# Kernel optimization log

Measured on AMD Instinct MI355X. Metric: run time of the kernel, lower is better.

## Reference

```python
import jax, jax.numpy as jnp
import numpy as np

D, ED, N, R, K, NL = 128, 256, 16, 8, 4, 3   # d_model, d_inner, d_state, dt_rank, d_conv, n_layers
B, L = 4, 1024
HID, OUT = 256, 2
EPS = 1e-5


def setup_inputs() -> dict:
    key = jax.random.key(0)
    ks = jax.random.split(key, 16)
    g = lambda k, shape, s=0.05: jax.random.normal(k, shape, dtype=jnp.float32) * s
    return {
        "x": jax.random.normal(ks[0], (B, L, D), dtype=jnp.float32),
        # Mamba params, stacked over (2 directions, NL layers)
        "rms_w": jnp.ones((2, NL, D), jnp.float32),
        "in_w": g(ks[1], (2, NL, 2 * ED, D)),
        "in_b": g(ks[2], (2, NL, 2 * ED)),
        "conv_w": g(ks[3], (2, NL, ED, K)),
        "conv_b": g(ks[4], (2, NL, ED)),
        "xproj_w": g(ks[5], (2, NL, R + 2 * N, ED)),
        "dt_w": g(ks[6], (2, NL, ED, R)),
        "dt_b": g(ks[7], (2, NL, ED)),
        "A_log": jnp.broadcast_to(jnp.log(jnp.arange(1.0, N + 1.0, dtype=jnp.float32)), (2, NL, ED, N)) + 0.0,
        "Dp": jnp.ones((2, NL, ED), jnp.float32),
        "out_w": g(ks[8], (2, NL, D, ED)),
        "out_b": g(ks[9], (2, NL, D)),
        # MLP head params (BatchNorm in training mode: batch stats)
        "bn1_g": jnp.ones((2 * D,), jnp.float32), "bn1_b": jnp.zeros((2 * D,), jnp.float32),
        "w1": g(ks[10], (HID, 2 * D)), "b1": g(ks[11], (HID,)),
        "bn2_g": jnp.ones((HID,), jnp.float32), "bn2_b": jnp.zeros((HID,), jnp.float32),
        "w2": g(ks[12], (HID, HID)), "b2": g(ks[13], (HID,)),
        "bn3_g": jnp.ones((HID,), jnp.float32), "bn3_b": jnp.zeros((HID,), jnp.float32),
        "w3": g(ks[14], (OUT, HID)), "b3": g(ks[15], (OUT,)),
    }


def _rms(x, w):
    return x * jax.lax.rsqrt(jnp.mean(x * x, axis=-1, keepdims=True) + EPS) * w


def _dwconv(x, w, b):
    # causal depthwise conv; x: (B,L,ED), w: (ED,K)
    y = jax.lax.conv_general_dilated(x.transpose(0, 2, 1), w[:, None, :], (1,), [(K - 1, 0)],
                                     feature_group_count=ED, dimension_numbers=("NCH", "OIH", "NCH"))
    return y.transpose(0, 2, 1) + b


def _ssm(dA, dBx, C):
    # dA,dBx: (B,L,ED,N); C: (B,L,N) -> y: (B,L,ED)
    def step(h, inp):
        a, bx, c = inp
        h = a * h + bx
        return h, jnp.einsum("ben,bn->be", h, c)
    h0 = jnp.zeros((dA.shape[0], ED, N), dA.dtype)
    _, ys = jax.lax.scan(step, h0, (dA.transpose(1, 0, 2, 3), dBx.transpose(1, 0, 2, 3), C.transpose(1, 0, 2)))
    return ys.transpose(1, 0, 2)


def _block(x, in_w, in_b, conv_w, conv_b, xproj_w, dt_w, dt_b, A_log, Dp, out_w, out_b):
    xz = x @ in_w.T + in_b
    xi, z = xz[..., :ED], xz[..., ED:]
    xi = jax.nn.silu(_dwconv(xi, conv_w, conv_b))
    dbc = xi @ xproj_w.T
    dt, Bm, Cm = dbc[..., :R], dbc[..., R:R + N], dbc[..., R + N:]
    delta = jax.nn.softplus(dt @ dt_w.T + dt_b)            # (B,L,ED)
    A = -jnp.exp(A_log)                                    # (ED,N)
    dA = jnp.exp(delta[..., None] * A)                     # (B,L,ED,N)
    dBx = (delta * xi)[..., None] * Bm[:, :, None, :]      # (B,L,ED,N)
    y = _ssm(dA, dBx, Cm) + Dp * xi
    y = y * jax.nn.silu(z)
    return y @ out_w.T + out_b


def _mamba(x, d, rms_w, in_w, in_b, conv_w, conv_b, xproj_w, dt_w, dt_b, A_log, Dp, out_w, out_b):
    for l in range(NL):
        x = x + _block(_rms(x, rms_w[d, l]), in_w[d, l], in_b[d, l], conv_w[d, l], conv_b[d, l],
                       xproj_w[d, l], dt_w[d, l], dt_b[d, l], A_log[d, l], Dp[d, l], out_w[d, l], out_b[d, l])
    return x


def _bn(x, g, b):
    m = jnp.mean(x, axis=0)
    v = jnp.mean((x - m) ** 2, axis=0)  # biased var, torch BN training mode
    return (x - m) * jax.lax.rsqrt(v + EPS) * g + b


def _forward(x, rms_w, in_w, in_b, conv_w, conv_b, xproj_w, dt_w, dt_b, A_log, Dp, out_w, out_b,
             bn1_g, bn1_b, w1, b1, bn2_g, bn2_b, w2, b2, bn3_g, bn3_b, w3, b3):
    mp = (rms_w, in_w, in_b, conv_w, conv_b, xproj_w, dt_w, dt_b, A_log, Dp, out_w, out_b)
    fwd = _mamba(x, 0, *mp)
    bwd = jnp.flip(_mamba(jnp.flip(x, axis=1), 1, *mp), axis=1)
    h = jnp.concatenate([fwd, bwd], axis=2).reshape(B * L, 2 * D)
    h = jax.nn.leaky_relu(_bn(h, bn1_g, bn1_b) @ w1.T + b1)
    h = jax.nn.leaky_relu(_bn(h, bn2_g, bn2_b) @ w2.T + b2)
    h = _bn(h, bn3_g, bn3_b) @ w3.T + b3
    return h.reshape(B, L, OUT)


def reference(x, rms_w, in_w, in_b, conv_w, conv_b, xproj_w, dt_w, dt_b, A_log, Dp, out_w, out_b,
              bn1_g, bn1_b, w1, b1, bn2_g, bn2_b, w2, b2, bn3_g, bn3_b, w3, b3):
    return _forward(x, rms_w, in_w, in_b, conv_w, conv_b, xproj_w, dt_w, dt_b, A_log, Dp, out_w, out_b,
                    bn1_g, bn1_b, w1, b1, bn2_g, bn2_b, w2, b2, bn3_g, bn3_b, w3, b3)
```

## Files before the change

kernel.cpp:

```cpp
#include <hip/hip_runtime.h>
#include <hip/hip_bf16.h>

#define NL 3
#define EPS 1e-5f

#define C_RMSW   0L
#define C_INW    768L
#define C_INB    393984L
#define C_CONVW  397056L
#define C_CONVB  403200L
#define C_XPROJW 404736L
#define C_DTW    466176L
#define C_DTB    478464L
#define C_ALOG   480000L
#define C_DP     504576L
#define C_OUTW   506112L
#define C_OUTB   702720L
#define C_BN1G   703488L
#define C_BN1B   703744L
#define C_W1     704000L
#define C_B1     769536L
#define C_BN2G   769792L
#define C_BN2B   770048L
#define C_W2     770304L
#define C_B2     835840L
#define C_BN3G   836096L
#define C_BN3B   836352L
#define C_W3     836608L
#define C_B3     837120L
#define FLAG_OFF 837184L
#define X0_OFF   837248L
#define X1_OFF   1361536L
#define XZT_OFF  1885824L
#define XCP_OFF  6080128L
#define DBCT_OFF 8177280L
#define YGP_OFF  8504960L
#define BNS_OFF  10602112L
#define H1_OFF   XZT_OFF
#define H2_OFF   (XZT_OFF + 1048576L)

struct Ptrs { const void* p[25]; };

static __device__ const int  CV_SRC[26] = {0,0,1,2,3,4,5,6,7,8,9,10,11,12,13,14,15,16,17,18,19,20,21,22,23,24};
static __device__ const long CV_DST[26] = {X0_OFF,X1_OFF,C_RMSW,C_INW,C_INB,C_CONVW,C_CONVB,C_XPROJW,C_DTW,C_DTB,
                                           C_ALOG,C_DP,C_OUTW,C_OUTB,C_BN1G,C_BN1B,C_W1,C_B1,C_BN2G,C_BN2B,
                                           C_W2,C_B2,C_BN3G,C_BN3B,C_W3,C_B3};
static __device__ const int  CV_SZ[26]  = {524288,524288,768,393216,3072,6144,1536,61440,12288,1536,
                                           24576,1536,196608,768,256,256,65536,256,256,256,
                                           65536,256,256,256,512,2};

__global__ __launch_bounds__(256) void k_convert(Ptrs ps, float* __restrict__ ws) {
  bool isbf = (*(const unsigned int*)ps.p[1]) == 0x3F803F80u;
  if (blockIdx.x == 0 && blockIdx.y == 0 && threadIdx.x == 0) ws[FLAG_OFF] = isbf ? 1.f : 0.f;
  int job = blockIdx.y;
  int n = CV_SZ[job];
  const void* s = ps.p[CV_SRC[job]];
  float* dp = ws + CV_DST[job];
  int stride = gridDim.x * blockDim.x;
  bool permute = (job < 2);
  for (int i = blockIdx.x * blockDim.x + threadIdx.x; i < n; i += stride) {
    long si = i;
    if (permute) {
      int row = i >> 7, col = i & 127;
      int b = row >> 10, p = row & 1023;
      int t = ((p & 63) << 4) + (p >> 6);
      si = ((long)((b << 10) + t) << 7) + col;
    }
    float v;
    if (isbf) {
      unsigned int u = ((const unsigned short*)s)[si];
      v = __uint_as_float(u << 16);
    } else {
      v = ((const float*)s)[si];
    }
    dp[i] = v;
  }
}

#define ASLD 68

__device__ inline void mm_inner(const float* As, const float* Bs, float4* acc) {
  int tx = threadIdx.x & 15, ty = threadIdx.x >> 4;
  #pragma unroll
  for (int k = 0; k < 64; ++k) {
    float4 av = *(const float4*)&As[k*ASLD + ty*4];
    float4 bv = *(const float4*)&Bs[k*ASLD + tx*4];
    acc[0].x = fmaf(av.x,bv.x,acc[0].x); acc[0].y = fmaf(av.x,bv.y,acc[0].y); acc[0].z = fmaf(av.x,bv.z,acc[0].z); acc[0].w = fmaf(av.x,bv.w,acc[0].w);
    acc[1].x = fmaf(av.y,bv.x,acc[1].x); acc[1].y = fmaf(av.y,bv.y,acc[1].y); acc[1].z = fmaf(av.y,bv.z,acc[1].z); acc[1].w = fmaf(av.y,bv.w,acc[1].w);
    acc[2].x = fmaf(av.z,bv.x,acc[2].x); acc[2].y = fmaf(av.z,bv.y,acc[2].y); acc[2].z = fmaf(av.z,bv.z,acc[2].z); acc[2].w = fmaf(av.z,bv.w,acc[2].w);
    acc[3].x = fmaf(av.w,bv.x,acc[3].x); acc[3].y = fmaf(av.w,bv.y,acc[3].y); acc[3].z = fmaf(av.w,bv.z,acc[3].z); acc[3].w = fmaf(av.w,bv.w,acc[3].w);
  }
}

__device__ inline void stageT_g(float* S, const float* src, int ld, int row0, int k0, int nvalid) {
  int m = threadIdx.x >> 2, q = threadIdx.x & 3;
  const float* p = src + (long)(row0 + m) * ld + k0 + q*16;
  bool ok = (row0 + m) < nvalid;
  #pragma unroll
  for (int j = 0; j < 4; ++j) {
    float4 v = ok ? *(const float4*)(p + j*4) : make_float4(0.f,0.f,0.f,0.f);
    int kk = q*16 + j*4;
    S[(kk+0)*ASLD+m] = v.x; S[(kk+1)*ASLD+m] = v.y; S[(kk+2)*ASLD+m] = v.z; S[(kk+3)*ASLD+m] = v.w;
  }
}

__device__ inline void stageD(float* S, const float* srcT, long ld, int m0, int k0) {
  int k = threadIdx.x >> 2, q = threadIdx.x & 3;
  const float* p = srcT + (long)(k0 + k) * ld + m0 + q*16;
  float4 v0 = *(const float4*)(p);
  float4 v1 = *(const float4*)(p+4);
  float4 v2 = *(const float4*)(p+8);
  float4 v3 = *(const float4*)(p+12);
  float* s = &S[k*ASLD + q*16];
  *(float4*)(s)    = v0; *(float4*)(s+4)  = v1; *(float4*)(s+8)  = v2; *(float4*)(s+12) = v3;
}

__global__ __launch_bounds__(256) void k1_rms_inproj(float* __restrict__ ws, int layer) {
  int d = blockIdx.z, mt = blockIdx.x, nt = blockIdx.y;
  const float* X  = ws + (d ? X1_OFF : X0_OFF);
  const float* W  = ws + C_INW + (long)((d*NL+layer)*512) * 128;
  const float* Rw = ws + C_RMSW + (d*NL+layer)*128;
  const float* Bi = ws + C_INB + (d*NL+layer)*512;
  __shared__ float As[64*ASLD];
  __shared__ float Bs[64*ASLD];
  __shared__ float rsq[64][4];
  __shared__ float rsc[64];
  int tx = threadIdx.x & 15, ty = threadIdx.x >> 4;
  float4 acc[4] = {make_float4(0,0,0,0),make_float4(0,0,0,0),make_float4(0,0,0,0),make_float4(0,0,0,0)};
  float sq = 0.f;
  for (int kt = 0; kt < 2; ++kt) {
    int k0 = kt * 64;
    {
      int m = threadIdx.x >> 2, q = threadIdx.x & 3;
      const float* p  = X + (long)(mt*64 + m) * 128 + k0 + q*16;
      const float* rw = Rw + k0 + q*16;
      #pragma unroll
      for (int j = 0; j < 4; ++j) {
        float4 v = *(const float4*)(p + j*4);
        float4 r = *(const float4*)(rw + j*4);
        sq += v.x*v.x + v.y*v.y + v.z*v.z + v.w*v.w;
        int kk = q*16 + j*4;
        As[(kk+0)*ASLD+m] = v.x*r.x; As[(kk+1)*ASLD+m] = v.y*r.y;
        As[(kk+2)*ASLD+m] = v.z*r.z; As[(kk+3)*ASLD+m] = v.w*r.w;
      }
    }
    stageT_g(Bs, W, 128, nt*64, k0, 512);
    __syncthreads();
    mm_inner(As, Bs, acc);
    __syncthreads();
  }
  { int m = threadIdx.x >> 2, q = threadIdx.x & 3; rsq[m][q] = sq; }
  __syncthreads();
  if (threadIdx.x < 64) {
    float s = rsq[threadIdx.x][0] + rsq[threadIdx.x][1] + rsq[threadIdx.x][2] + rsq[threadIdx.x][3];
    rsc[threadIdx.x] = rsqrtf(s * (1.f/128.f) + EPS);
  }
  __syncthreads();
  int n0 = tx*4;
  float4 bb = *(const float4*)&Bi[nt*64 + n0];
  const float* bbp = (const float*)&bb;
  #pragma unroll
  for (int i = 0; i < 4; ++i) {
    int m = ty*4 + i;
    float r = rsc[m];
    const float* av = (const float*)&acc[i];
    #pragma unroll
    for (int cc = 0; cc < 4; ++cc) {
      As[(n0+cc)*65 + m] = av[cc]*r + bbp[cc];
    }
  }
  __syncthreads();
  float* xzt = ws + XZT_OFF + (long)d*2097152L + (long)(nt*64)*4096 + mt*64;
  #pragma unroll
  for (int r = 0; r < 16; ++r) {
    int el = r*256 + threadIdx.x;
    int row = el >> 6, m = el & 63;
    xzt[(long)row*4096 + m] = As[row*65 + m];
  }
}

__global__ __launch_bounds__(256) void k2_conv(float* __restrict__ ws, int layer) {
  int e = blockIdx.x, d = blockIdx.y;
  const float* xrow = ws + XZT_OFF + (long)d*2097152L + (long)e*4096;
  float* orow = ws + XCP_OFF + (long)d*1048576L + (long)e*4096;
  __shared__ float s1[4*1040];
  __shared__ float s2[4*1040];
  int tid = threadIdx.x;
  #pragma unroll
  for (int r = 0; r < 16; ++r) {
    int g = r*256 + tid;
    int b = g >> 10, p = g & 1023;
    int s = (p >> 6)*65 + (p & 63);
    s1[b*1040 + s] = xrow[g];
  }
  __syncthreads();
  float4 wv = *(const float4*)(ws + C_CONVW + (long)((d*NL+layer)*256 + e) * 4);
  float cb = ws[C_CONVB + (d*NL+layer)*256 + e];
  #pragma unroll
  for (int r = 0; r < 16; ++r) {
    int tg = r*256 + tid;
    int b = tg >> 10, tl = tg & 1023;
    const float* st = s1 + b*1040;
    #define SIDX(t) (((t)&15)*65 + ((t)>>4))
    float a = cb;
    if (d == 0) {
      float x0 = (tl >= 3) ? st[SIDX(tl-3)] : 0.f;
      float x1 = (tl >= 2) ? st[SIDX(tl-2)] : 0.f;
      float x2 = (tl >= 1) ? st[SIDX(tl-1)] : 0.f;
      float x3 = st[SIDX(tl)];
      a += wv.x*x0 + wv.y*x1 + wv.z*x2 + wv.w*x3;
    } else {
      float x0 = (tl <= 1020) ? st[SIDX(tl+3)] : 0.f;
      float x1 = (tl <= 1021) ? st[SIDX(tl+2)] : 0.f;
      float x2 = (tl <= 1022) ? st[SIDX(tl+1)] : 0.f;
      float x3 = st[SIDX(tl)];
      a += wv.x*x0 + wv.y*x1 + wv.z*x2 + wv.w*x3;
    }
    #undef SIDX
    s2[b*1040 + ((tl & 15)*65 + (tl >> 4))] = a / (1.f + __expf(-a));
  }
  __syncthreads();
  #pragma unroll
  for (int r = 0; r < 16; ++r) {
    int g = r*256 + tid;
    int b = g >> 10, p = g & 1023;
    orow[g] = s2[b*1040 + (p >> 6)*65 + (p & 63)];
  }
}

__global__ __launch_bounds__(256) void k3_xproj(float* __restrict__ ws, int layer) {
  int d = blockIdx.z, mt = blockIdx.x;
  int m0 = mt * 64;
  const float* srcT = ws + XCP_OFF + (long)d*1048576L;
  const float* W = ws + C_XPROJW + (long)((d*NL+layer)*40) * 256;
  __shared__ float As[64*ASLD];
  __shared__ float Bs[64*ASLD];
  float4 acc[4] = {make_float4(0,0,0,0),make_float4(0,0,0,0),make_float4(0,0,0,0),make_float4(0,0,0,0)};
  for (int kt = 0; kt < 4; ++kt) {
    stageD(As, srcT, 4096L, m0, kt*64);
    stageT_g(Bs, W, 256, 0, kt*64, 40);
    __syncthreads();
    mm_inner(As, Bs, acc);
    __syncthreads();
  }
  int tx = threadIdx.x & 15, ty = threadIdx.x >> 4;
  #pragma unroll
  for (int i = 0; i < 4; ++i) {
    const float* av = (const float*)&acc[i];
    #pragma unroll
    for (int cc = 0; cc < 4; ++cc) {
      Bs[(tx*4+cc)*65 + ty*4+i] = av[cc];
    }
  }
  __syncthreads();
  float* dbcT = ws + DBCT_OFF + (long)d*163840L;
  #pragma unroll
  for (int r = 0; r < 10; ++r) {
    int el = r*256 + threadIdx.x;
    int n = el >> 6, m = el & 63;
    dbcT[(long)n*4096 + m0 + m] = Bs[n*65 + m];
  }
}

__device__ inline float softplusf(float x) {
  if (x > 20.f) return x;
  return __logf(1.f + __expf(x));
}

__global__ __launch_bounds__(256) void k5_scan(float* __restrict__ ws, int layer) {
  int d = blockIdx.z, b = blockIdx.y, eg = blockIdx.x;
  int es = threadIdx.x >> 6;
  int c  = threadIdx.x & 63;
  int e = eg*4 + es;
  int g0 = b*1024 + c;
  const float* xcp = ws + XCP_OFF + (long)d*1048576L + (long)e*4096 + g0;
  const float* zp  = ws + XZT_OFF + (long)d*2097152L + (long)(256+e)*4096 + g0;
  const float* dbc = ws + DBCT_OFF + (long)d*163840L + g0;
  float*       yo  = ws + YGP_OFF + (long)d*1048576L + (long)e*4096 + g0;
  const float* dw = ws + C_DTW + (long)((d*NL+layer)*256 + e)*8;
  float dtb = ws[C_DTB + (d*NL+layer)*256 + e];
  const float* al = ws + C_ALOG + (long)((d*NL+layer)*256 + e)*16;
  float Dpe = ws[C_DP + (d*NL+layer)*256 + e];
  float dtw[8];
  #pragma unroll
  for (int n = 0; n < 8; ++n) dtw[n] = dw[n];
  float Anv[16]; bool fast = true;
  #pragma unroll
  for (int n = 0; n < 16; ++n) {
    Anv[n] = -__expf(al[n]);
    fast = fast && (fabsf(Anv[n] + (float)(n+1)) < 1e-3f * (float)(n+1));
  }
  __shared__ float aL[4*64*17];
  __shared__ float hL[4*64*17];
  float h[16], ap[16], del[16], xcv[16];
  float Q = 1.f;
  #pragma unroll
  for (int n = 0; n < 16; ++n) { h[n] = 0.f; ap[n] = 1.f; }
  int i0 = d ? 15 : 0, di = d ? -1 : 1;
  for (int s = 0; s < 16; ++s) {
    int i = i0 + s*di;
    int off = i*64;
    float a0 = dtb;
    #pragma unroll
    for (int n = 0; n < 8; ++n) a0 += dbc[(long)n*4096 + off] * dtw[n];
    float dl = softplusf(a0);
    float xc = xcp[off];
    del[s] = dl; xcv[s] = xc;
    float dx = dl * xc;
    if (fast) {
      float q = __expf(-dl);
      float qp[16];
      qp[0]=q; qp[1]=q*q; qp[2]=qp[1]*q; qp[3]=qp[1]*qp[1];
      float q4=qp[3];
      qp[4]=qp[0]*q4; qp[5]=qp[1]*q4; qp[6]=qp[2]*q4; qp[7]=q4*q4;
      float q8=qp[7];
      #pragma unroll
      for (int j = 0; j < 8; ++j) qp[8+j]=qp[j]*q8;
      Q *= q;
      #pragma unroll
      for (int n = 0; n < 16; ++n)
        h[n] = fmaf(qp[n], h[n], dx * dbc[(long)(8+n)*4096 + off]);
    } else {
      #pragma unroll
      for (int n = 0; n < 16; ++n) {
        float a = __expf(dl * Anv[n]);
        ap[n] *= a;
        h[n] = fmaf(a, h[n], dx * dbc[(long)(8+n)*4096 + off]);
      }
    }
  }
  if (fast) {
    float p = Q;
    #pragma unroll
    for (int n = 0; n < 16; ++n) { ap[n] = p; p *= Q; }
  }
  int base = (es*64 + c)*17;
  #pragma unroll
  for (int n = 0; n < 16; ++n) { aL[base+n] = ap[n]; hL[base+n] = h[n]; }
  __syncthreads();
  if (threadIdx.x < 64) {
    int e2 = threadIdx.x >> 4, n = threadIdx.x & 15;
    float h0 = 0.f;
    for (int s2 = 0; s2 < 64; ++s2) {
      int cc = d ? (63 - s2) : s2;
      int ix = (e2*64 + cc)*17 + n;
      float ta = aL[ix], th = hL[ix];
      aL[ix] = h0;
      h0 = fmaf(ta, h0, th);
    }
  }
  __syncthreads();
  #pragma unroll
  for (int n = 0; n < 16; ++n) h[n] = aL[base+n];
  for (int s = 0; s < 16; ++s) {
    int i = i0 + s*di;
    int off = i*64;
    float dl = del[s], xc = xcv[s];
    float dx = dl * xc;
    float zr = zp[off];
    float zg = zr / (1.f + __expf(-zr));
    float ya[4] = {0.f,0.f,0.f,0.f};
    if (fast) {
      float q = __expf(-dl);
      float qp[16];
      qp[0]=q; qp[1]=q*q; qp[2]=qp[1]*q; qp[3]=qp[1]*qp[1];
      float q4=qp[3];
      qp[4]=qp[0]*q4; qp[5]=qp[1]*q4; qp[6]=qp[2]*q4; qp[7]=q4*q4;
      float q8=qp[7];
      #pragma unroll
      for (int j = 0; j < 8; ++j) qp[8+j]=qp[j]*q8;
      #pragma unroll
      for (int n = 0; n < 16; ++n) {
        h[n] = fmaf(qp[n], h[n], dx * dbc[(long)(8+n)*4096 + off]);
        ya[n & 3] = fmaf(h[n], dbc[(long)(24+n)*4096 + off], ya[n & 3]);
      }
    } else {
      #pragma unroll
      for (int n = 0; n < 16; ++n) {
        float a = __expf(dl * Anv[n]);
        h[n] = fmaf(a, h[n], dx * dbc[(long)(8+n)*4096 + off]);
        ya[n & 3] = fmaf(h[n], dbc[(long)(24+n)*4096 + off], ya[n & 3]);
      }
    }
    float y = (ya[0] + ya[1]) + (ya[2] + ya[3]);
    y = fmaf(Dpe, xc, y);
    yo[off] = y * zg;
  }
}

__global__ __launch_bounds__(256) void k6_outproj(float* __restrict__ ws, int layer) {
  int d = blockIdx.z, mt = blockIdx.x, nt = blockIdx.y;
  int m0 = mt * 64;
  const float* srcT = ws + YGP_OFF + (long)d*1048576L;
  const float* W  = ws + C_OUTW + (long)((d*NL+layer)*128) * 256;
  const float* Ob = ws + C_OUTB + (d*NL+layer)*128;
  float* Xd = ws + (d ? X1_OFF : X0_OFF);
  __shared__ float As[64*ASLD];
  __shared__ float Bs[64*ASLD];
  float4 acc[4] = {make_float4(0,0,0,0),make_float4(0,0,0,0),make_float4(0,0,0,0),make_float4(0,0,0,0)};
  for (int kt = 0; kt < 4; ++kt) {
    stageD(As, srcT, 4096L, m0, kt*64);
    stageT_g(Bs, W, 256, nt*64, kt*64, 128);
    __syncthreads();
    mm_inner(As, Bs, acc);
    __syncthreads();
  }
  int tx = threadIdx.x & 15, ty = threadIdx.x >> 4;
  int n0 = nt*64 + tx*4;
  float4 ob4 = *(const float4*)&Ob[n0];
  #pragma unroll
  for (int i = 0; i < 4; ++i) {
    long tok = (long)m0 + ty*4 + i;
    float4 cur = *(float4*)&Xd[tok*128 + n0];
    float4 v;
    v.x = acc[i].x + ob4.x + cur.x; v.y = acc[i].y + ob4.y + cur.y;
    v.z = acc[i].z + ob4.z + cur.z; v.w = acc[i].w + ob4.w + cur.w;
    *(float4*)&Xd[tok*128 + n0] = v;
  }
}

__global__ __launch_bounds__(256) void bn_stats(float* __restrict__ ws, int stage) {
  int ch = blockIdx.x;
  const float* src; long ld; const float* g; const float* bb;
  if (stage == 0) { src = ws + ((ch < 128) ? (X0_OFF + ch) : (X1_OFF + ch - 128)); ld = 128; g = ws + C_BN1G; bb = ws + C_BN1B; }
  else if (stage == 1) { src = ws + H1_OFF + ch; ld = 256; g = ws + C_BN2G; bb = ws + C_BN2B; }
  else { src = ws + H2_OFF + ch; ld = 256; g = ws + C_BN3G; bb = ws + C_BN3B; }
  float s = 0.f, s2 = 0.f;
  for (int i = threadIdx.x; i < 4096; i += 256) {
    float v = src[(long)i * ld];
    s += v; s2 += v*v;
  }
  #pragma unroll
  for (int o = 32; o > 0; o >>= 1) { s += __shfl_down(s, o, 64); s2 += __shfl_down(s2, o, 64); }
  __shared__ float ls[4], ls2[4];
  int wid = threadIdx.x >> 6, lane = threadIdx.x & 63;
  if (lane == 0) { ls[wid] = s; ls2[wid] = s2; }
  __syncthreads();
  if (threadIdx.x == 0) {
    float S = ls[0]+ls[1]+ls[2]+ls[3], S2 = ls2[0]+ls2[1]+ls2[2]+ls2[3];
    float mean = S * (1.f/4096.f);
    float var = S2 * (1.f/4096.f) - mean*mean;
    float sc = g[ch] * rsqrtf(var + EPS);
    ws[BNS_OFF + stage*512 + ch] = sc;
    ws[BNS_OFF + stage*512 + 256 + ch] = bb[ch] - mean * sc;
  }
}

template<int STAGE>
__global__ __launch_bounds__(256) void hgemm_k(float* __restrict__ ws, void* dout) {
  int mt = blockIdx.x, nt = blockIdx.y;
  const float* sc = ws + BNS_OFF + STAGE*512;
  const float* sh = sc + 256;
  const float* W = ws + (STAGE == 0 ? C_W1 : (STAGE == 1 ? C_W2 : C_W3));
  __shared__ float As[64*ASLD];
  __shared__ float Bs[64*ASLD];
  float4 acc[4] = {make_float4(0,0,0,0),make_float4(0,0,0,0),make_float4(0,0,0,0),make_float4(0,0,0,0)};
  for (int kt = 0; kt < 4; ++kt) {
    int k0 = kt * 64;
    const float* src; int ld;
    if (STAGE == 0) { ld = 128; src = (k0 < 128) ? (ws + X0_OFF + k0) : (ws + X1_OFF + (k0 - 128)); }
    else { ld = 256; src = ws + (STAGE == 1 ? H1_OFF : H2_OFF) + k0; }
    {
      int m = threadIdx.x >> 2, q = threadIdx.x & 3;
      const float* p   = src + (long)(mt*64 + m) * ld + q*16;
      const float* scp = sc + k0 + q*16;
      const float* shp = sh + k0 + q*16;
      #pragma unroll
      for (int j = 0; j < 4; ++j) {
        float4 v  = *(const float4*)(p + j*4);
        float4 s4 = *(const float4*)(scp + j*4);
        float4 h4 = *(const float4*)(shp + j*4);
        int kk = q*16 + j*4;
        As[(kk+0)*ASLD+m] = v.x*s4.x + h4.x; As[(kk+1)*ASLD+m] = v.y*s4.y + h4.y;
        As[(kk+2)*ASLD+m] = v.z*s4.z + h4.z; As[(kk+3)*ASLD+m] = v.w*s4.w + h4.w;
      }
    }
    stageT_g(Bs, W, 256, nt*64, k0, STAGE == 2 ? 2 : 256);
    __syncthreads();
    mm_inner(As, Bs, acc);
    __syncthreads();
  }
  int tx = threadIdx.x & 15, ty = threadIdx.x >> 4;
  if (STAGE == 2) {
    if (tx == 0) {
      bool isbf = ws[FLAG_OFF] != 0.f;
      float b0 = ws[C_B3], b1 = ws[C_B3 + 1];
      #pragma unroll
      for (int i = 0; i < 4; ++i) {
        int r = mt*64 + ty*4 + i;
        int b = r >> 10, p = r & 1023;
        int t = ((p & 63) << 4) + (p >> 6);
        long tok = (long)(b << 10) + t;
        float v0 = acc[i].x + b0, v1 = acc[i].y + b1;
        if (isbf) {
          __hip_bfloat16* o = (__hip_bfloat16*)dout;
          o[tok*2]   = __float2bfloat16(v0);
          o[tok*2+1] = __float2bfloat16(v1);
        } else {
          float* o = (float*)dout;
          o[tok*2] = v0; o[tok*2+1] = v1;
        }
      }
    }
  } else {
    const float* bp = ws + (STAGE == 0 ? C_B1 : C_B2);
    int n0 = nt*64 + tx*4;
    float4 b4 = *(const float4*)&bp[n0];
    float* H = ws + (STAGE == 0 ? H1_OFF : H2_OFF);
    #pragma unroll
    for (int i = 0; i < 4; ++i) {
      long tok = (long)mt*64 + ty*4 + i;
      float4 v;
      v.x = acc[i].x + b4.x; v.y = acc[i].y + b4.y; v.z = acc[i].z + b4.z; v.w = acc[i].w + b4.w;
      v.x = v.x > 0.f ? v.x : 0.01f*v.x;
      v.y = v.y > 0.f ? v.y : 0.01f*v.y;
      v.z = v.z > 0.f ? v.z : 0.01f*v.z;
      v.w = v.w > 0.f ? v.w : 0.01f*v.w;
      *(float4*)&H[tok*256 + n0] = v;
    }
  }
}

extern "C" void kernel_launch(void* const* d_in, const int* in_sizes, int n_in,
                              void* d_out, int out_size, void* d_ws, size_t ws_size,
                              hipStream_t stream) {
  (void)in_sizes; (void)n_in; (void)out_size; (void)ws_size;
  float* ws = (float*)d_ws;
  Ptrs ps;
  for (int i = 0; i < 25; ++i) ps.p[i] = d_in[i];
  k_convert<<<dim3(64, 26), dim3(256), 0, stream>>>(ps, ws);
  for (int l = 0; l < NL; ++l) {
    k1_rms_inproj<<<dim3(64, 8, 2), dim3(256), 0, stream>>>(ws, l);
    k2_conv      <<<dim3(256, 2),   dim3(256), 0, stream>>>(ws, l);
    k3_xproj     <<<dim3(64, 1, 2), dim3(256), 0, stream>>>(ws, l);
    k5_scan      <<<dim3(64, 4, 2), dim3(256), 0, stream>>>(ws, l);
    k6_outproj   <<<dim3(64, 2, 2), dim3(256), 0, stream>>>(ws, l);
  }
  bn_stats<<<dim3(256), dim3(256), 0, stream>>>(ws, 0);
  hgemm_k<0><<<dim3(64, 4), dim3(256), 0, stream>>>(ws, d_out);
  bn_stats<<<dim3(256), dim3(256), 0, stream>>>(ws, 1);
  hgemm_k<1><<<dim3(64, 4), dim3(256), 0, stream>>>(ws, d_out);
  bn_stats<<<dim3(256), dim3(256), 0, stream>>>(ws, 2);
  hgemm_k<2><<<dim3(64, 1), dim3(256), 0, stream>>>(ws, d_out);
}
```

Before: 463.9 us.

## Use fp16 MFMA for projections and fuse BatchNorm stats into GEMM epilogues

The in-projection, out-projection and two MLP head GEMMs now run on fp16 MFMA 16x16x32 instructions instead of scalar fp32 FMA tiles. Weights are pre-converted to fp16 once, with the RMSNorm weight folded into the in-projection weights. BatchNorm batch statistics are accumulated with atomics in the producing GEMM epilogues, which removes the separate bn_stats kernels. In exchange, fp16 rounding of activations and weights reduces accuracy, and variance computed as E[x^2]-mean^2 with float atomics is less stable and not bit-reproducible.

```diff
diff --git a/kernel.cpp b/kernel.cpp
--- a/kernel.cpp
+++ b/kernel.cpp
@@ -1,11 +1,10 @@
 #include <hip/hip_runtime.h>
 #include <hip/hip_bf16.h>
+#include <hip/hip_fp16.h>
 
 #define NL 3
 #define EPS 1e-5f
 
-#define C_RMSW   0L
-#define C_INW    768L
 #define C_INB    393984L
 #define C_CONVW  397056L
 #define C_CONVB  403200L
@@ -14,15 +13,12 @@
 #define C_DTB    478464L
 #define C_ALOG   480000L
 #define C_DP     504576L
-#define C_OUTW   506112L
 #define C_OUTB   702720L
 #define C_BN1G   703488L
 #define C_BN1B   703744L
-#define C_W1     704000L
 #define C_B1     769536L
 #define C_BN2G   769792L
 #define C_BN2B   770048L
-#define C_W2     770304L
 #define C_B2     835840L
 #define C_BN3G   836096L
 #define C_BN3B   836352L
@@ -35,49 +31,77 @@
 #define XCP_OFF  6080128L
 #define DBCT_OFF 8177280L
 #define YGP_OFF  8504960L
-#define BNS_OFF  10602112L
+#define BNA_OFF  10603648L
+#define HINW_OFF  10605184L
+#define HOUTW_OFF 10801792L
+#define HW1_OFF   10900096L
+#define HW2_OFF   10932864L
 #define H1_OFF   XZT_OFF
 #define H2_OFF   (XZT_OFF + 1048576L)
 
+#define ASLD 68
+
 struct Ptrs { const void* p[25]; };
 
-static __device__ const int  CV_SRC[26] = {0,0,1,2,3,4,5,6,7,8,9,10,11,12,13,14,15,16,17,18,19,20,21,22,23,24};
-static __device__ const long CV_DST[26] = {X0_OFF,X1_OFF,C_RMSW,C_INW,C_INB,C_CONVW,C_CONVB,C_XPROJW,C_DTW,C_DTB,
-                                           C_ALOG,C_DP,C_OUTW,C_OUTB,C_BN1G,C_BN1B,C_W1,C_B1,C_BN2G,C_BN2B,
-                                           C_W2,C_B2,C_BN3G,C_BN3B,C_W3,C_B3};
-static __device__ const int  CV_SZ[26]  = {524288,524288,768,393216,3072,6144,1536,61440,12288,1536,
-                                           24576,1536,196608,768,256,256,65536,256,256,256,
-                                           65536,256,256,256,512,2};
-
-__global__ __launch_bounds__(256) void k_convert(Ptrs ps, float* __restrict__ ws) {
+typedef _Float16 half8 __attribute__((ext_vector_type(8)));
+typedef float f32x4 __attribute__((ext_vector_type(4)));
+
+static __device__ const int  CV_SRC[21] = {0,0,3,4,5,6,7,8,9,10,12,13,14,16,17,18,20,21,22,23,24};
+static __device__ const long CV_DST[21] = {X0_OFF,X1_OFF,C_INB,C_CONVW,C_CONVB,C_XPROJW,C_DTW,C_DTB,C_ALOG,C_DP,
+                                           C_OUTB,C_BN1G,C_BN1B,C_B1,C_BN2G,C_BN2B,C_B2,C_BN3G,C_BN3B,C_W3,C_B3};
+static __device__ const int  CV_SZ[21]  = {524288,524288,3072,6144,1536,61440,12288,1536,24576,1536,
+                                           768,256,256,256,256,256,256,256,256,512,2};
+
+__device__ inline float ldsrc(const void* s, long i, bool isbf) {
+  if (isbf) { unsigned int u = ((const unsigned short*)s)[i]; return __uint_as_float(u << 16); }
+  return ((const float*)s)[i];
+}
+
+__global__ __launch_bounds__(256) void g_convert(Ptrs ps, float* __restrict__ ws) {
   bool isbf = (*(const unsigned int*)ps.p[1]) == 0x3F803F80u;
-  if (blockIdx.x == 0 && blockIdx.y == 0 && threadIdx.x == 0) ws[FLAG_OFF] = isbf ? 1.f : 0.f;
   int job = blockIdx.y;
-  int n = CV_SZ[job];
-  const void* s = ps.p[CV_SRC[job]];
-  float* dp = ws + CV_DST[job];
-  int stride = gridDim.x * blockDim.x;
-  bool permute = (job < 2);
-  for (int i = blockIdx.x * blockDim.x + threadIdx.x; i < n; i += stride) {
-    long si = i;
-    if (permute) {
-      int row = i >> 7, col = i & 127;
-      int b = row >> 10, p = row & 1023;
-      int t = ((p & 63) << 4) + (p >> 6);
-      si = ((long)((b << 10) + t) << 7) + col;
-    }
-    float v;
-    if (isbf) {
-      unsigned int u = ((const unsigned short*)s)[si];
-      v = __uint_as_float(u << 16);
-    } else {
-      v = ((const float*)s)[si];
-    }
-    dp[i] = v;
-  }
-}
-
-#define ASLD 68
+  if (job == 0 && blockIdx.x == 0 && threadIdx.x == 0) ws[FLAG_OFF] = isbf ? 1.f : 0.f;
+  int tid0 = blockIdx.x * 256 + threadIdx.x;
+  int stride = gridDim.x * 256;
+  if (job < 21) {
+    int n = CV_SZ[job];
+    const void* s = ps.p[CV_SRC[job]];
+    float* dp = ws + CV_DST[job];
+    bool permute = (job < 2);
+    for (int i = tid0; i < n; i += stride) {
+      long si = i;
+      if (permute) {
+        int row = i >> 7, col = i & 127;
+        int b = row >> 10, p = row & 1023;
+        int t = ((p & 63) << 4) + (p >> 6);
+        si = ((long)((b << 10) + t) << 7) + col;
+      }
+      dp[i] = ldsrc(s, si, isbf);
+    }
+  } else if (job == 21) {
+    _Float16* dp = (_Float16*)(ws + HINW_OFF);
+    const void* sw = ps.p[2]; const void* sr = ps.p[1];
+    for (int i = tid0; i < 393216; i += stride) {
+      int dl = i >> 16, k = i & 127;
+      float v = ldsrc(sw, i, isbf) * ldsrc(sr, dl*128 + k, isbf);
+      dp[i] = (_Float16)v;
+    }
+  } else if (job == 22) {
+    _Float16* dp = (_Float16*)(ws + HOUTW_OFF);
+    const void* s = ps.p[11];
+    for (int i = tid0; i < 196608; i += stride) dp[i] = (_Float16)ldsrc(s, i, isbf);
+  } else if (job == 23) {
+    _Float16* dp = (_Float16*)(ws + HW1_OFF);
+    const void* s = ps.p[15];
+    for (int i = tid0; i < 65536; i += stride) dp[i] = (_Float16)ldsrc(s, i, isbf);
+  } else if (job == 24) {
+    _Float16* dp = (_Float16*)(ws + HW2_OFF);
+    const void* s = ps.p[19];
+    for (int i = tid0; i < 65536; i += stride) dp[i] = (_Float16)ldsrc(s, i, isbf);
+  } else {
+    for (int i = tid0; i < 1536; i += stride) ws[BNA_OFF + i] = 0.f;
+  }
+}
 
 __device__ inline void mm_inner(const float* As, const float* Bs, float4* acc) {
   int tx = threadIdx.x & 15, ty = threadIdx.x >> 4;
@@ -115,71 +139,72 @@
   *(float4*)(s)    = v0; *(float4*)(s+4)  = v1; *(float4*)(s+8)  = v2; *(float4*)(s+12) = v3;
 }
 
-__global__ __launch_bounds__(256) void k1_rms_inproj(float* __restrict__ ws, int layer) {
-  int d = blockIdx.z, mt = blockIdx.x, nt = blockIdx.y;
-  const float* X  = ws + (d ? X1_OFF : X0_OFF);
-  const float* W  = ws + C_INW + (long)((d*NL+layer)*512) * 128;
-  const float* Rw = ws + C_RMSW + (d*NL+layer)*128;
+__device__ inline float softplusf(float x) {
+  if (x > 20.f) return x;
+  return __logf(1.f + __expf(x));
+}
+
+__global__ __launch_bounds__(256) void g_k1m(float* __restrict__ ws, int layer) {
+  int d = blockIdx.z, nt = blockIdx.y, pt = blockIdx.x;
+  const float* X = ws + (d ? X1_OFF : X0_OFF);
+  const _Float16* Wf = (const _Float16*)(ws + HINW_OFF) + (long)(d*NL+layer)*65536;
   const float* Bi = ws + C_INB + (d*NL+layer)*512;
-  __shared__ float As[64*ASLD];
-  __shared__ float Bs[64*ASLD];
-  __shared__ float rsq[64][4];
+  __shared__ float rsq[256];
   __shared__ float rsc[64];
-  int tx = threadIdx.x & 15, ty = threadIdx.x >> 4;
-  float4 acc[4] = {make_float4(0,0,0,0),make_float4(0,0,0,0),make_float4(0,0,0,0),make_float4(0,0,0,0)};
-  float sq = 0.f;
-  for (int kt = 0; kt < 2; ++kt) {
-    int k0 = kt * 64;
-    {
-      int m = threadIdx.x >> 2, q = threadIdx.x & 3;
-      const float* p  = X + (long)(mt*64 + m) * 128 + k0 + q*16;
-      const float* rw = Rw + k0 + q*16;
-      #pragma unroll
-      for (int j = 0; j < 4; ++j) {
-        float4 v = *(const float4*)(p + j*4);
-        float4 r = *(const float4*)(rw + j*4);
-        sq += v.x*v.x + v.y*v.y + v.z*v.z + v.w*v.w;
-        int kk = q*16 + j*4;
-        As[(kk+0)*ASLD+m] = v.x*r.x; As[(kk+1)*ASLD+m] = v.y*r.y;
-        As[(kk+2)*ASLD+m] = v.z*r.z; As[(kk+3)*ASLD+m] = v.w*r.w;
-      }
-    }
-    stageT_g(Bs, W, 128, nt*64, k0, 512);
-    __syncthreads();
-    mm_inner(As, Bs, acc);
-    __syncthreads();
-  }
-  { int m = threadIdx.x >> 2, q = threadIdx.x & 3; rsq[m][q] = sq; }
+  int p0 = pt*64;
+  {
+    int row = threadIdx.x >> 2, q = threadIdx.x & 3;
+    const float* xp = X + (long)(p0+row)*128 + q*32;
+    float s = 0.f;
+    #pragma unroll
+    for (int j = 0; j < 8; ++j) {
+      float4 v = *(const float4*)(xp + j*4);
+      s += v.x*v.x + v.y*v.y + v.z*v.z + v.w*v.w;
+    }
+    rsq[row*4+q] = s;
+  }
   __syncthreads();
   if (threadIdx.x < 64) {
-    float s = rsq[threadIdx.x][0] + rsq[threadIdx.x][1] + rsq[threadIdx.x][2] + rsq[threadIdx.x][3];
+    float s = rsq[threadIdx.x*4] + rsq[threadIdx.x*4+1] + rsq[threadIdx.x*4+2] + rsq[threadIdx.x*4+3];
     rsc[threadIdx.x] = rsqrtf(s * (1.f/128.f) + EPS);
   }
   __syncthreads();
-  int n0 = tx*4;
-  float4 bb = *(const float4*)&Bi[nt*64 + n0];
-  const float* bbp = (const float*)&bb;
-  #pragma unroll
-  for (int i = 0; i < 4; ++i) {
-    int m = ty*4 + i;
-    float r = rsc[m];
-    const float* av = (const float*)&acc[i];
-    #pragma unroll
-    for (int cc = 0; cc < 4; ++cc) {
-      As[(n0+cc)*65 + m] = av[cc]*r + bbp[cc];
-    }
-  }
-  __syncthreads();
-  float* xzt = ws + XZT_OFF + (long)d*2097152L + (long)(nt*64)*4096 + mt*64;
-  #pragma unroll
-  for (int r = 0; r < 16; ++r) {
-    int el = r*256 + threadIdx.x;
-    int row = el >> 6, m = el & 63;
-    xzt[(long)row*4096 + m] = As[row*65 + m];
-  }
-}
-
-__global__ __launch_bounds__(256) void k2_conv(float* __restrict__ ws, int layer) {
+  int w = threadIdx.x >> 6, lane = threadIdx.x & 63;
+  int quad = lane >> 4, lm = lane & 15;
+  int n0 = nt*64 + w*16;
+  f32x4 zero = {0.f,0.f,0.f,0.f};
+  f32x4 acc[4] = {zero, zero, zero, zero};
+  #pragma unroll
+  for (int s = 0; s < 4; ++s) {
+    int k0 = s*32 + quad*8;
+    half8 af = *(const half8*)(Wf + (long)(n0+lm)*128 + k0);
+    #pragma unroll
+    for (int t = 0; t < 4; ++t) {
+      int pr = t*16 + lm;
+      const float* xp = X + (long)(p0+pr)*128 + k0;
+      float4 v0 = *(const float4*)xp;
+      float4 v1 = *(const float4*)(xp+4);
+      float r = rsc[pr];
+      half8 bf;
+      bf[0]=(_Float16)(v0.x*r); bf[1]=(_Float16)(v0.y*r); bf[2]=(_Float16)(v0.z*r); bf[3]=(_Float16)(v0.w*r);
+      bf[4]=(_Float16)(v1.x*r); bf[5]=(_Float16)(v1.y*r); bf[6]=(_Float16)(v1.z*r); bf[7]=(_Float16)(v1.w*r);
+      acc[t] = __builtin_amdgcn_mfma_f32_16x16x32_f16(af, bf, acc[t], 0, 0, 0);
+    }
+  }
+  float* xzt = ws + XZT_OFF + (long)d*2097152L;
+  #pragma unroll
+  for (int r = 0; r < 4; ++r) {
+    int n = n0 + quad*4 + r;
+    float bias = Bi[n];
+    #pragma unroll
+    for (int t = 0; t < 4; ++t) {
+      int p = p0 + t*16 + lm;
+      xzt[(long)n*4096 + p] = acc[t][r] + bias;
+    }
+  }
+}
+
+__global__ __launch_bounds__(256) void g_k2(float* __restrict__ ws, int layer) {
   int e = blockIdx.x, d = blockIdx.y;
   const float* xrow = ws + XZT_OFF + (long)d*2097152L + (long)e*4096;
   float* orow = ws + XCP_OFF + (long)d*1048576L + (long)e*4096;
@@ -228,7 +253,7 @@
   }
 }
 
-__global__ __launch_bounds__(256) void k3_xproj(float* __restrict__ ws, int layer) {
+__global__ __launch_bounds__(256) void g_k3(float* __restrict__ ws, int layer) {
   int d = blockIdx.z, mt = blockIdx.x;
   int m0 = mt * 64;
   const float* srcT = ws + XCP_OFF + (long)d*1048576L;
@@ -262,12 +287,7 @@
   }
 }
 
-__device__ inline float softplusf(float x) {
-  if (x > 20.f) return x;
-  return __logf(1.f + __expf(x));
-}
-
-__global__ __launch_bounds__(256) void k5_scan(float* __restrict__ ws, int layer) {
+__global__ __launch_bounds__(256) void g_k5(float* __restrict__ ws, int layer) {
   int d = blockIdx.z, b = blockIdx.y, eg = blockIdx.x;
   int es = threadIdx.x >> 6;
   int c  = threadIdx.x & 63;
@@ -388,135 +408,189 @@
   }
 }
 
-__global__ __launch_bounds__(256) void k6_outproj(float* __restrict__ ws, int layer) {
-  int d = blockIdx.z, mt = blockIdx.x, nt = blockIdx.y;
-  int m0 = mt * 64;
-  const float* srcT = ws + YGP_OFF + (long)d*1048576L;
-  const float* W  = ws + C_OUTW + (long)((d*NL+layer)*128) * 256;
+__global__ __launch_bounds__(256) void g_k6m(float* __restrict__ ws, int layer) {
+  int d = blockIdx.z, pt = blockIdx.x;
+  int p0 = pt*16;
+  const float* Y = ws + YGP_OFF + (long)d*1048576L;
+  const _Float16* Wf = (const _Float16*)(ws + HOUTW_OFF) + (long)(d*NL+layer)*32768;
   const float* Ob = ws + C_OUTB + (d*NL+layer)*128;
   float* Xd = ws + (d ? X1_OFF : X0_OFF);
+  __shared__ __align__(16) _Float16 Ah[16*264];
+  {
+    int e = threadIdx.x;
+    const float* yp = Y + (long)e*4096 + p0;
+    float4 v0 = *(const float4*)yp;
+    float4 v1 = *(const float4*)(yp+4);
+    float4 v2 = *(const float4*)(yp+8);
+    float4 v3 = *(const float4*)(yp+12);
+    float vv[16] = {v0.x,v0.y,v0.z,v0.w, v1.x,v1.y,v1.z,v1.w,
+                    v2.x,v2.y,v2.z,v2.w, v3.x,v3.y,v3.z,v3.w};
+    #pragma unroll
+    for (int p = 0; p < 16; ++p) Ah[p*264 + e] = (_Float16)vv[p];
+  }
+  __syncthreads();
+  int w = threadIdx.x >> 6, lane = threadIdx.x & 63;
+  int quad = lane >> 4, lm = lane & 15;
+  f32x4 zero = {0.f,0.f,0.f,0.f};
+  f32x4 acc[2] = {zero, zero};
+  #pragma unroll
+  for (int s = 0; s < 8; ++s) {
+    int k0 = s*32 + quad*8;
+    half8 af = *(const half8*)(&Ah[lm*264 + k0]);
+    #pragma unroll
+    for (int t = 0; t < 2; ++t) {
+      int n = w*32 + t*16 + lm;
+      half8 bf = *(const half8*)(Wf + (long)n*256 + k0);
+      acc[t] = __builtin_amdgcn_mfma_f32_16x16x32_f16(af, bf, acc[t], 0, 0, 0);
+    }
+  }
+  bool dostats = (layer == NL-1);
+  float* bna = ws + BNA_OFF;
+  #pragma unroll
+  for (int t = 0; t < 2; ++t) {
+    int n = w*32 + t*16 + lm;
+    float ob = Ob[n];
+    float s1 = 0.f, s2 = 0.f;
+    #pragma unroll
+    for (int r = 0; r < 4; ++r) {
+      int p = p0 + quad*4 + r;
+      float v = acc[t][r] + ob + Xd[(long)p*128 + n];
+      Xd[(long)p*128 + n] = v;
+      s1 += v; s2 += v*v;
+    }
+    if (dostats) {
+      s1 += __shfl_xor(s1, 16, 64); s2 += __shfl_xor(s2, 16, 64);
+      s1 += __shfl_xor(s1, 32, 64); s2 += __shfl_xor(s2, 32, 64);
+      if (quad == 0) {
+        int ch = d*128 + n;
+        atomicAdd(&bna[ch], s1);
+        atomicAdd(&bna[256 + ch], s2);
+      }
+    }
+  }
+}
+
+template<int STAGE>
+__global__ __launch_bounds__(256) void g_hgm(float* __restrict__ ws) {
+  int p0 = blockIdx.x * 16;
+  __shared__ float scL[256], shL[256];
+  {
+    int k = threadIdx.x;
+    float S = ws[BNA_OFF + STAGE*512 + k], S2 = ws[BNA_OFF + STAGE*512 + 256 + k];
+    float mean = S * (1.f/4096.f);
+    float var = S2 * (1.f/4096.f) - mean*mean;
+    const float* g = ws + (STAGE == 0 ? C_BN1G : C_BN2G);
+    const float* bb = ws + (STAGE == 0 ? C_BN1B : C_BN2B);
+    float sc = g[k] * rsqrtf(var + EPS);
+    scL[k] = sc; shL[k] = bb[k] - mean*sc;
+  }
+  __syncthreads();
+  const _Float16* Wf = (const _Float16*)(ws + (STAGE == 0 ? HW1_OFF : HW2_OFF));
+  const float* bias = ws + (STAGE == 0 ? C_B1 : C_B2);
+  float* H = ws + (STAGE == 0 ? H1_OFF : H2_OFF);
+  int w = threadIdx.x >> 6, lane = threadIdx.x & 63;
+  int quad = lane >> 4, lm = lane & 15;
+  f32x4 zero = {0.f,0.f,0.f,0.f};
+  f32x4 acc[4] = {zero, zero, zero, zero};
+  #pragma unroll
+  for (int s = 0; s < 8; ++s) {
+    int k0 = s*32 + quad*8;
+    const float* src;
+    if (STAGE == 0) src = (k0 < 128) ? (ws + X0_OFF + (long)(p0+lm)*128 + k0)
+                                     : (ws + X1_OFF + (long)(p0+lm)*128 + (k0-128));
+    else            src = ws + H1_OFF + (long)(p0+lm)*256 + k0;
+    float4 v0 = *(const float4*)src, v1 = *(const float4*)(src+4);
+    float4 c0 = *(const float4*)&scL[k0], c1 = *(const float4*)&scL[k0+4];
+    float4 h0 = *(const float4*)&shL[k0], h1 = *(const float4*)&shL[k0+4];
+    half8 af;
+    af[0]=(_Float16)(v0.x*c0.x+h0.x); af[1]=(_Float16)(v0.y*c0.y+h0.y);
+    af[2]=(_Float16)(v0.z*c0.z+h0.z); af[3]=(_Float16)(v0.w*c0.w+h0.w);
+    af[4]=(_Float16)(v1.x*c1.x+h1.x); af[5]=(_Float16)(v1.y*c1.y+h1.y);
+    af[6]=(_Float16)(v1.z*c1.z+h1.z); af[7]=(_Float16)(v1.w*c1.w+h1.w);
+    #pragma unroll
+    for (int t = 0; t < 4; ++t) {
+      int n = w*64 + t*16 + lm;
+      half8 bf = *(const half8*)(Wf + (long)n*256 + k0);
+      acc[t] = __builtin_amdgcn_mfma_f32_16x16x32_f16(af, bf, acc[t], 0, 0, 0);
+    }
+  }
+  float* bna = ws + BNA_OFF + (STAGE+1)*512;
+  #pragma unroll
+  for (int t = 0; t < 4; ++t) {
+    int n = w*64 + t*16 + lm;
+    float bs = bias[n];
+    float s1 = 0.f, s2 = 0.f;
+    #pragma unroll
+    for (int r = 0; r < 4; ++r) {
+      int p = p0 + quad*4 + r;
+      float v = acc[t][r] + bs;
+      v = v > 0.f ? v : 0.01f*v;
+      H[(long)p*256 + n] = v;
+      s1 += v; s2 += v*v;
+    }
+    s1 += __shfl_xor(s1, 16, 64); s2 += __shfl_xor(s2, 16, 64);
+    s1 += __shfl_xor(s1, 32, 64); s2 += __shfl_xor(s2, 32, 64);
+    if (quad == 0) {
+      atomicAdd(&bna[n], s1);
+      atomicAdd(&bna[256 + n], s2);
+    }
+  }
+}
+
+__global__ __launch_bounds__(256) void g_hg2(float* __restrict__ ws, void* dout) {
+  int mt = blockIdx.x;
   __shared__ float As[64*ASLD];
   __shared__ float Bs[64*ASLD];
-  float4 acc[4] = {make_float4(0,0,0,0),make_float4(0,0,0,0),make_float4(0,0,0,0),make_float4(0,0,0,0)};
-  for (int kt = 0; kt < 4; ++kt) {
-    stageD(As, srcT, 4096L, m0, kt*64);
-    stageT_g(Bs, W, 256, nt*64, kt*64, 128);
-    __syncthreads();
-    mm_inner(As, Bs, acc);
-    __syncthreads();
-  }
-  int tx = threadIdx.x & 15, ty = threadIdx.x >> 4;
-  int n0 = nt*64 + tx*4;
-  float4 ob4 = *(const float4*)&Ob[n0];
-  #pragma unroll
-  for (int i = 0; i < 4; ++i) {
-    long tok = (long)m0 + ty*4 + i;
-    float4 cur = *(float4*)&Xd[tok*128 + n0];
-    float4 v;
-    v.x = acc[i].x + ob4.x + cur.x; v.y = acc[i].y + ob4.y + cur.y;
-    v.z = acc[i].z + ob4.z + cur.z; v.w = acc[i].w + ob4.w + cur.w;
-    *(float4*)&Xd[tok*128 + n0] = v;
-  }
-}
-
-__global__ __launch_bounds__(256) void bn_stats(float* __restrict__ ws, int stage) {
-  int ch = blockIdx.x;
-  const float* src; long ld; const float* g; const float* bb;
-  if (stage == 0) { src = ws + ((ch < 128) ? (X0_OFF + ch) : (X1_OFF + ch - 128)); ld = 128; g = ws + C_BN1G; bb = ws + C_BN1B; }
-  else if (stage == 1) { src = ws + H1_OFF + ch; ld = 256; g = ws + C_BN2G; bb = ws + C_BN2B; }
-  else { src = ws + H2_OFF + ch; ld = 256; g = ws + C_BN3G; bb = ws + C_BN3B; }
-  float s = 0.f, s2 = 0.f;
-  for (int i = threadIdx.x; i < 4096; i += 256) {
-    float v = src[(long)i * ld];
-    s += v; s2 += v*v;
-  }
-  #pragma unroll
-  for (int o = 32; o > 0; o >>= 1) { s += __shfl_down(s, o, 64); s2 += __shfl_down(s2, o, 64); }
-  __shared__ float ls[4], ls2[4];
-  int wid = threadIdx.x >> 6, lane = threadIdx.x & 63;
-  if (lane == 0) { ls[wid] = s; ls2[wid] = s2; }
-  __syncthreads();
-  if (threadIdx.x == 0) {
-    float S = ls[0]+ls[1]+ls[2]+ls[3], S2 = ls2[0]+ls2[1]+ls2[2]+ls2[3];
+  __shared__ float scL[256], shL[256];
+  {
+    int k = threadIdx.x;
+    float S = ws[BNA_OFF + 2*512 + k], S2 = ws[BNA_OFF + 2*512 + 256 + k];
     float mean = S * (1.f/4096.f);
     float var = S2 * (1.f/4096.f) - mean*mean;
-    float sc = g[ch] * rsqrtf(var + EPS);
-    ws[BNS_OFF + stage*512 + ch] = sc;
-    ws[BNS_OFF + stage*512 + 256 + ch] = bb[ch] - mean * sc;
-  }
-}
-
-template<int STAGE>
-__global__ __launch_bounds__(256) void hgemm_k(float* __restrict__ ws, void* dout) {
-  int mt = blockIdx.x, nt = blockIdx.y;
-  const float* sc = ws + BNS_OFF + STAGE*512;
-  const float* sh = sc + 256;
-  const float* W = ws + (STAGE == 0 ? C_W1 : (STAGE == 1 ? C_W2 : C_W3));
-  __shared__ float As[64*ASLD];
-  __shared__ float Bs[64*ASLD];
+    float sc = ws[C_BN3G + k] * rsqrtf(var + EPS);
+    scL[k] = sc; shL[k] = ws[C_BN3B + k] - mean*sc;
+  }
+  __syncthreads();
   float4 acc[4] = {make_float4(0,0,0,0),make_float4(0,0,0,0),make_float4(0,0,0,0),make_float4(0,0,0,0)};
   for (int kt = 0; kt < 4; ++kt) {
     int k0 = kt * 64;
-    const float* src; int ld;
-    if (STAGE == 0) { ld = 128; src = (k0 < 128) ? (ws + X0_OFF + k0) : (ws + X1_OFF + (k0 - 128)); }
-    else { ld = 256; src = ws + (STAGE == 1 ? H1_OFF : H2_OFF) + k0; }
     {
       int m = threadIdx.x >> 2, q = threadIdx.x & 3;
-      const float* p   = src + (long)(mt*64 + m) * ld + q*16;
-      const float* scp = sc + k0 + q*16;
-      const float* shp = sh + k0 + q*16;
+      const float* p = ws + H2_OFF + (long)(mt*64 + m)*256 + k0 + q*16;
       #pragma unroll
       for (int j = 0; j < 4; ++j) {
         float4 v  = *(const float4*)(p + j*4);
-        float4 s4 = *(const float4*)(scp + j*4);
-        float4 h4 = *(const float4*)(shp + j*4);
+        float4 s4 = *(const float4*)&scL[k0 + q*16 + j*4];
+        float4 h4 = *(const float4*)&shL[k0 + q*16 + j*4];
         int kk = q*16 + j*4;
         As[(kk+0)*ASLD+m] = v.x*s4.x + h4.x; As[(kk+1)*ASLD+m] = v.y*s4.y + h4.y;
         As[(kk+2)*ASLD+m] = v.z*s4.z + h4.z; As[(kk+3)*ASLD+m] = v.w*s4.w + h4.w;
       }
     }
-    stageT_g(Bs, W, 256, nt*64, k0, STAGE == 2 ? 2 : 256);
+    stageT_g(Bs, ws + C_W3, 256, 0, k0, 2);
     __syncthreads();
     mm_inner(As, Bs, acc);
     __syncthreads();
   }
   int tx = threadIdx.x & 15, ty = threadIdx.x >> 4;
-  if (STAGE == 2) {
-    if (tx == 0) {
-      bool isbf = ws[FLAG_OFF] != 0.f;
-      float b0 = ws[C_B3], b1 = ws[C_B3 + 1];
-      #pragma unroll
-      for (int i = 0; i < 4; ++i) {
-        int r = mt*64 + ty*4 + i;
-        int b = r >> 10, p = r & 1023;
-        int t = ((p & 63) << 4) + (p >> 6);
-        long tok = (long)(b << 10) + t;
-        float v0 = acc[i].x + b0, v1 = acc[i].y + b1;
-        if (isbf) {
-          __hip_bfloat16* o = (__hip_bfloat16*)dout;
-          o[tok*2]   = __float2bfloat16(v0);
-          o[tok*2+1] = __float2bfloat16(v1);
-        } else {
-          float* o = (float*)dout;
-          o[tok*2] = v0; o[tok*2+1] = v1;
-        }
+  if (tx == 0) {
+    bool isbf = ws[FLAG_OFF] != 0.f;
+    float b0 = ws[C_B3], b1 = ws[C_B3 + 1];
+    #pragma unroll
+    for (int i = 0; i < 4; ++i) {
+      int r = mt*64 + ty*4 + i;
+      int b = r >> 10, p = r & 1023;
+      int t = ((p & 63) << 4) + (p >> 6);
+      long tok = (long)(b << 10) + t;
+      float v0 = acc[i].x + b0, v1 = acc[i].y + b1;
+      if (isbf) {
+        __hip_bfloat16* o = (__hip_bfloat16*)dout;
+        o[tok*2]   = __float2bfloat16(v0);
+        o[tok*2+1] = __float2bfloat16(v1);
+      } else {
+        float* o = (float*)dout;
+        o[tok*2] = v0; o[tok*2+1] = v1;
       }
-    }
-  } else {
-    const float* bp = ws + (STAGE == 0 ? C_B1 : C_B2);
-    int n0 = nt*64 + tx*4;
-    float4 b4 = *(const float4*)&bp[n0];
-    float* H = ws + (STAGE == 0 ? H1_OFF : H2_OFF);
-    #pragma unroll
-    for (int i = 0; i < 4; ++i) {
-      long tok = (long)mt*64 + ty*4 + i;
-      float4 v;
-      v.x = acc[i].x + b4.x; v.y = acc[i].y + b4.y; v.z = acc[i].z + b4.z; v.w = acc[i].w + b4.w;
-      v.x = v.x > 0.f ? v.x : 0.01f*v.x;
-      v.y = v.y > 0.f ? v.y : 0.01f*v.y;
-      v.z = v.z > 0.f ? v.z : 0.01f*v.z;
-      v.w = v.w > 0.f ? v.w : 0.01f*v.w;
-      *(float4*)&H[tok*256 + n0] = v;
     }
   }
 }
@@ -528,18 +602,15 @@
   float* ws = (float*)d_ws;
   Ptrs ps;
   for (int i = 0; i < 25; ++i) ps.p[i] = d_in[i];
-  k_convert<<<dim3(64, 26), dim3(256), 0, stream>>>(ps, ws);
+  g_convert<<<dim3(32, 26), dim3(256), 0, stream>>>(ps, ws);
   for (int l = 0; l < NL; ++l) {
-    k1_rms_inproj<<<dim3(64, 8, 2), dim3(256), 0, stream>>>(ws, l);
-    k2_conv      <<<dim3(256, 2),   dim3(256), 0, stream>>>(ws, l);
-    k3_xproj     <<<dim3(64, 1, 2), dim3(256), 0, stream>>>(ws, l);
-    k5_scan      <<<dim3(64, 4, 2), dim3(256), 0, stream>>>(ws, l);
-    k6_outproj   <<<dim3(64, 2, 2), dim3(256), 0, stream>>>(ws, l);
-  }
-  bn_stats<<<dim3(256), dim3(256), 0, stream>>>(ws, 0);
-  hgemm_k<0><<<dim3(64, 4), dim3(256), 0, stream>>>(ws, d_out);
-  bn_stats<<<dim3(256), dim3(256), 0, stream>>>(ws, 1);
-  hgemm_k<1><<<dim3(64, 4), dim3(256), 0, stream>>>(ws, d_out);
-  bn_stats<<<dim3(256), dim3(256), 0, stream>>>(ws, 2);
-  hgemm_k<2><<<dim3(64, 1), dim3(256), 0, stream>>>(ws, d_out);
-}
+    g_k1m<<<dim3(64, 8, 2), dim3(256), 0, stream>>>(ws, l);
+    g_k2 <<<dim3(256, 2),   dim3(256), 0, stream>>>(ws, l);
+    g_k3 <<<dim3(64, 1, 2), dim3(256), 0, stream>>>(ws, l);
+    g_k5 <<<dim3(64, 4, 2), dim3(256), 0, stream>>>(ws, l);
+    g_k6m<<<dim3(256, 1, 2), dim3(256), 0, stream>>>(ws, l);
+  }
+  g_hgm<0><<<dim3(256), dim3(256), 0, stream>>>(ws);
+  g_hgm<1><<<dim3(256), dim3(256), 0, stream>>>(ws);
+  g_hg2<<<dim3(64), dim3(256), 0, stream>>>(ws, d_out);
+}
```

Result: faster. 433.6 us (-6.5%).
